# Kernel optimization log

Measured on AMD Instinct MI355X. Metric: run time of the kernel, lower is better.

Reference implementation:

```python
import jax, jax.numpy as jnp
import numpy as np

D_MODEL = 1024
NUM_HEADS = 16
HEAD_DIM = D_MODEL // NUM_HEADS
B, S = 2, 2048
EPS = 1e-8


def setup_inputs() -> dict:
    key = jax.random.key(0)
    ks = jax.random.split(key, 9)
    sc = 1.0 / np.sqrt(D_MODEL)
    return {
        "x": jax.random.normal(ks[0], (B, S, D_MODEL), jnp.float32),
        "wq": jax.random.normal(ks[1], (D_MODEL, D_MODEL), jnp.float32) * sc,
        "bq": jax.random.normal(ks[2], (D_MODEL,), jnp.float32) * 0.01,
        "wk": jax.random.normal(ks[3], (D_MODEL, D_MODEL), jnp.float32) * sc,
        "bk": jax.random.normal(ks[4], (D_MODEL,), jnp.float32) * 0.01,
        "wv": jax.random.normal(ks[5], (D_MODEL, D_MODEL), jnp.float32) * sc,
        "bv": jax.random.normal(ks[6], (D_MODEL,), jnp.float32) * 0.01,
        "wo": jax.random.normal(ks[7], (D_MODEL, D_MODEL), jnp.float32) * sc,
        "bo": jax.random.normal(ks[8], (D_MODEL,), jnp.float32) * 0.01,
    }


def reference(x, wq, bq, wk, bk, wv, bv, wo, bo):
    b, s, d = x.shape
    h, hd = NUM_HEADS, HEAD_DIM
    # projections (torch Linear: y = x W^T + b); reshape to [b, h, s, hd]
    def proj(w, bias):
        return (jnp.einsum('bsd,ed->bse', x, w) + bias).reshape(b, s, h, hd).transpose(0, 2, 1, 3)
    q = proj(wq, bq)
    k = proj(wk, bk)
    v = proj(wv, bv)
    scores = jnp.einsum('bhqd,bhkd->bhqk', q, k) / np.sqrt(hd)
    attn = jax.nn.softmax(scores, axis=-1)
    o = jnp.einsum('bhqk,bhkd->bhqd', attn, v)  # [b, h, s, hd]
    # per-position, per-head Gram-Schmidt exclusion: remove component of o[i]
    # along v[i] (the loop in the original is independent over positions)
    v_norm_sq = jnp.sum(v * v, axis=-1, keepdims=True)          # [b,h,s,1]
    align = jnp.sum(o * v, axis=-1, keepdims=True) / (v_norm_sq + EPS)
    o = o - align * v
    o = o.transpose(0, 2, 1, 3).reshape(b, s, d)
    return jnp.einsum('bsd,ed->bse', o, wo) + bo
```

## Files before the change

kernel.cpp:

```cpp
#include <hip/hip_runtime.h>
#include <stdint.h>

#define SEQ 2048
#define NTOK 4096
#define DM 1024

typedef __bf16 bf16x8 __attribute__((ext_vector_type(8)));
typedef __bf16 bf16x4 __attribute__((ext_vector_type(4)));
typedef float f32x4 __attribute__((ext_vector_type(4)));

__device__ __forceinline__ unsigned short f2bf(float f) {
  union { float f; unsigned u; } v; v.f = f;
  return (unsigned short)((v.u + 0x7fffu + ((v.u >> 16) & 1u)) >> 16);
}
__device__ __forceinline__ float bf2f(unsigned short s) {
  union { unsigned u; float f; } v; v.u = ((unsigned)s) << 16; return v.f;
}
__device__ __forceinline__ unsigned pkbf(float a, float b) {
  union { float f; unsigned u; } x, y; x.f = a; y.f = b;
  return __builtin_amdgcn_perm(y.u + 0x8000u, x.u + 0x8000u, 0x07060302u);
}

__device__ __forceinline__ void async16(const unsigned short* g, unsigned short* l) {
  __builtin_amdgcn_global_load_lds(
      (const __attribute__((address_space(1))) void*)g,
      (__attribute__((address_space(3))) void*)l, 16, 0, 0);
}

__global__ __launch_bounds__(256) void cast_all(
    const float* __restrict__ x, const float* __restrict__ wq,
    const float* __restrict__ wk, const float* __restrict__ wv,
    const float* __restrict__ wo, unsigned short* __restrict__ dst) {
  size_t i = ((size_t)blockIdx.x * 256 + threadIdx.x) * 4;
  const float* src; size_t off;
  if (i < (size_t)NTOK * DM) { src = x; off = i; }
  else {
    size_t j = i - (size_t)NTOK * DM;
    int s = (int)(j >> 20);
    src = (s == 0) ? wq : (s == 1) ? wk : (s == 2) ? wv : wo;
    off = j & 1048575u;
  }
  float4 f = *(const float4*)(src + off);
  ushort4 o;
  o.x = f2bf(f.x); o.y = f2bf(f.y); o.z = f2bf(f.z); o.w = f2bf(f.w);
  *(ushort4*)(dst + i) = o;
}


template<int MI>
__device__ __forceinline__ void stage_half(
    const unsigned short* __restrict__ A, const unsigned short* __restrict__ Bw,
    int m0, int n0, int kt, unsigned short* As, unsigned short* Bs) {
  const int tid = threadIdx.x;
  const int r = tid >> 2, c = tid & 3;
#pragma unroll
  for (int b = 0; b < MI / 2; ++b) {
    const int row = b * 64 + r;
    async16(A + (size_t)(m0 + row) * 1024 + kt + ((c ^ (row & 3)) << 3),
            As + row * 32 + c * 8);
  }
#pragma unroll
  for (int b = 0; b < 2; ++b) {
    const int row = b * 64 + r;
    async16(Bw + (size_t)(n0 + row) * 1024 + kt + ((c ^ (row & 3)) << 3),
            Bs + row * 32 + c * 8);
  }
}

__device__ __forceinline__ void pipe_bar0() {
  asm volatile("s_waitcnt vmcnt(0)\ns_barrier" ::: "memory");
}
template<int MI>
__device__ __forceinline__ void pipe_barN() {
  if constexpr (MI == 4) asm volatile("s_waitcnt vmcnt(4)\ns_barrier" ::: "memory");
  else                   asm volatile("s_waitcnt vmcnt(3)\ns_barrier" ::: "memory");
}

template<int MI>
__device__ __forceinline__ void gemm_pipe(
    const unsigned short* __restrict__ A, const unsigned short* __restrict__ Bw,
    int m0, int n0, f32x4 (&acc)[MI][4],
    unsigned short* AsBase, unsigned short* BsBase) {
  const int tid = threadIdx.x, lane = tid & 63, w = tid >> 6;
  const int wm16 = (w >> 1) * MI * 16, wn = (w & 1) * 64;
  const int quad = lane >> 4, l16 = lane & 15;
  constexpr int ASZ = MI * 32 * 32;
  constexpr int BSZ = 128 * 32;

  stage_half<MI>(A, Bw, m0, n0, 0,  AsBase,       BsBase);
  stage_half<MI>(A, Bw, m0, n0, 32, AsBase + ASZ, BsBase + BSZ);
  pipe_barN<MI>();

  int cur = 0;
  for (int p = 0; p < 32; ++p) {
    const unsigned short* As = AsBase + cur * ASZ;
    const unsigned short* Bs = BsBase + cur * BSZ;

    bf16x8 af[MI], bf[4];
    const int swz = ((quad ^ (l16 & 3)) << 3);
#pragma unroll
    for (int i = 0; i < MI; ++i)
      af[i] = *(const bf16x8*)(As + (wm16 + i * 16 + l16) * 32 + swz);
#pragma unroll
    for (int j = 0; j < 4; ++j)
      bf[j] = *(const bf16x8*)(Bs + (wn + j * 16 + l16) * 32 + swz);

    if (p + 2 < 32) {
      const int slot = (cur == 0) ? 2 : cur - 1;
      stage_half<MI>(A, Bw, m0, n0, (p + 2) * 32,
                     AsBase + slot * ASZ, BsBase + slot * BSZ);
    }

#pragma unroll
    for (int i = 0; i < MI; ++i)
#pragma unroll
      for (int j = 0; j < 4; ++j)
        acc[i][j] = __builtin_amdgcn_mfma_f32_16x16x32_bf16(af[i], bf[j], acc[i][j], 0, 0, 0);

    if (p < 30)       pipe_barN<MI>();
    else if (p == 30) pipe_bar0();
    cur = (cur == 2) ? 0 : cur + 1;
  }
}

__global__ __launch_bounds__(256, 3) void qkv_gemm(
    const unsigned short* __restrict__ xb,
    const unsigned short* __restrict__ wqb, const unsigned short* __restrict__ wkb,
    const unsigned short* __restrict__ wvb,
    const float* __restrict__ bq, const float* __restrict__ bk, const float* __restrict__ bv,
    unsigned short* __restrict__ Q, unsigned short* __restrict__ Kd,
    unsigned short* __restrict__ Vt) {
  __shared__ unsigned short As[3 * 128 * 32], Bs[3 * 128 * 32];
  const int gx = blockIdx.x;
  const int kind = gx >> 8;
  const int rr = gx & 255;
  const int tok = 4 * (rr & 7) + ((rr >> 3) & 3);
  const int oth = rr >> 5;
  const unsigned short* A; const unsigned short* Bw;
  int m0, n0;
  if (kind == 2) { A = wvb; Bw = xb; m0 = oth * 128; n0 = tok * 128; }
  else { A = xb; Bw = kind ? wkb : wqb; m0 = tok * 128; n0 = oth * 128; }

  f32x4 acc[4][4];
#pragma unroll
  for (int i = 0; i < 4; ++i)
#pragma unroll
    for (int j = 0; j < 4; ++j) { f32x4 z = {0.f, 0.f, 0.f, 0.f}; acc[i][j] = z; }
  gemm_pipe<4>(A, Bw, m0, n0, acc, As, Bs);

  const int lane = threadIdx.x & 63, w = threadIdx.x >> 6;
  const int quad = lane >> 4, l16 = lane & 15;
  const int wm = (w >> 1) * 64, wn = (w & 1) * 64;

  if (kind == 2) {
#pragma unroll
    for (int i = 0; i < 4; ++i)
#pragma unroll
      for (int j = 0; j < 4; ++j) {
        const int n = n0 + wn + j * 16 + l16;
        const int tb = n >> 11, s = n & 2047;
#pragma unroll
        for (int r = 0; r < 4; ++r) {
          const int m = m0 + wm + i * 16 + quad * 4 + r;
          const int h = m >> 6, d = m & 63;
          Vt[((size_t)(tb * 16 + h) * 64 + d) * SEQ + s] = f2bf(acc[i][j][r] + bv[m]);
        }
      }
  } else {
    const float* bias = (kind == 0) ? bq : bk;
    const float scale = (kind == 0) ? 0.180336880f : 1.0f;
#pragma unroll
    for (int i = 0; i < 4; ++i)
#pragma unroll
    for (int j = 0; j < 4; ++j) {
        const int col = n0 + wn + j * 16 + l16;
        const float bb = bias[col];
        const int h = col >> 6, d = col & 63;
#pragma unroll
        for (int r = 0; r < 4; ++r) {
          const int m = m0 + wm + i * 16 + quad * 4 + r;
          const int b = m >> 11, s = m & 2047;
          const int bh = b * 16 + h;
          const unsigned short val = f2bf((acc[i][j][r] + bb) * scale);
          if (kind == 0) Q[((size_t)bh * SEQ + s) * 64 + d] = val;
          else           Kd[((size_t)bh * SEQ + s) * 64 + d] = val;
        }
      }
  }
}

__global__ __launch_bounds__(256, 2) void attn_kernel(
    const unsigned short* __restrict__ Q, const unsigned short* __restrict__ Kd,
    const unsigned short* __restrict__ Vt,
    unsigned short* __restrict__ O) {
  __shared__ unsigned short SH[32768];
#define KKB(g, b) (SH + ((g) * 2 + (b)) * 4096)
#define VVB(g, b) (SH + 16384 + ((g) * 2 + (b)) * 4096)
  const int gx = blockIdx.x;
  const int xcd = gx & 7;
  const int idx = gx >> 3;
  const int bh  = xcd * 4 + (idx & 3);
  const int q0  = (idx >> 2) * 128;
  const int tid = threadIdx.x, lane = tid & 63, w = tid >> 6;
  const int kp = w >> 1;
  const int wq = w & 1;
  const int quad = lane >> 4, l16 = lane & 15;
  const unsigned short* Qp = Q + (size_t)bh * SEQ * 64;
  const unsigned short* Kp = Kd + (size_t)bh * SEQ * 64;
  const unsigned short* Vp = Vt + (size_t)bh * 64 * SEQ;
  const int srow = tid >> 3;
  const int sc = ((tid & 7) ^ ((srow & 3) | ((srow & 8) >> 1))) << 3;

#pragma unroll
  for (int c = 0; c < 4; ++c)
    async16(Qp + (size_t)(q0 + c * 32 + srow) * 64 + sc,
            KKB(0, c >> 1) + (c & 1) * 2048 + tid * 8);
  __syncthreads();

  const int gl = (l16 & 3) | ((l16 & 8) >> 1);
  const int sel = l16 & 7;
  const unsigned short* Qsrc = KKB(0, wq);
  bf16x8 bQ[4][2];
#pragma unroll
  for (int qq = 0; qq < 4; ++qq) {
    const int qrow = qq * 16 + l16;
#pragma unroll
    for (int hh = 0; hh < 2; ++hh)
      bQ[qq][hh] = *(const bf16x8*)(Qsrc + qrow * 64 + (((hh * 4 + quad) ^ gl) << 3));
  }
  __syncthreads();

  auto stageKV = [&](int it_, int nb) {
#pragma unroll
    for (int g = 0; g < 2; ++g) {
      const int kt = g * 1024 + it_ * 64;
      async16(Kp + (size_t)(kt + srow) * 64 + sc, KKB(g, nb) + tid * 8);
      async16(Kp + (size_t)(kt + 32 + srow) * 64 + sc, KKB(g, nb) + 2048 + tid * 8);
      async16(Vp + (size_t)srow * SEQ + kt + sc, VVB(g, nb) + tid * 8);
      async16(Vp + (size_t)(32 + srow) * SEQ + kt + sc, VVB(g, nb) + 2048 + tid * 8);
    }
  };
  stageKV(0, 0);

  union { unsigned short u[8]; bf16x8 v; } one8;
#pragma unroll
  for (int t = 0; t < 8; ++t) one8.u[t] = 0x3F80;
  const bf16x8 aOnes = one8.v;

  f32x4 o_acc[4][4];
  f32x4 l_acc[4];
  const f32x4 zinit = {-12.f, -12.f, -12.f, -12.f};
#pragma unroll
  for (int qq = 0; qq < 4; ++qq) {
    f32x4 z = {0.f, 0.f, 0.f, 0.f};
    l_acc[qq] = z;
#pragma unroll
    for (int dt = 0; dt < 4; ++dt) o_acc[qq][dt] = z;
  }

  for (int it = 0; it < 16; ++it) {
    const int cur = it & 1;
    __syncthreads();
    if (it + 1 < 16) stageKV(it + 1, (it + 1) & 1);
    const unsigned short* Ks = KKB(kp, cur);
    const unsigned short* Vs = VVB(kp, cur);

    __builtin_amdgcn_s_setprio(1);

    bf16x8 bP[4][2];
#pragma unroll
    for (int ee = 0; ee < 4; ++ee) {
      const int G = ee >> 1, e = ee & 1;
      const int R = G * 32 + ((l16 >> 2) << 3) + e * 4 + (l16 & 3);
      const unsigned short* arow = Ks + R * 64;
      bf16x8 a0 = *(const bf16x8*)(arow + ((quad ^ sel) << 3));
      bf16x8 a1 = *(const bf16x8*)(arow + (((4 + quad) ^ sel) << 3));
#pragma unroll
      for (int qq = 0; qq < 4; ++qq) {
        f32x4 z = __builtin_amdgcn_mfma_f32_16x16x32_bf16(a0, bQ[qq][0], zinit, 0, 0, 0);
        z = __builtin_amdgcn_mfma_f32_16x16x32_bf16(a1, bQ[qq][1], z, 0, 0, 0);
        const unsigned u0 = (unsigned)(int)__builtin_fmaf(z[0], 8388608.0f, 1065024977.0f);
        const unsigned u1 = (unsigned)(int)__builtin_fmaf(z[1], 8388608.0f, 1065024977.0f);
        const unsigned u2 = (unsigned)(int)__builtin_fmaf(z[2], 8388608.0f, 1065024977.0f);
        const unsigned u3 = (unsigned)(int)__builtin_fmaf(z[3], 8388608.0f, 1065024977.0f);
        union { unsigned d[4]; bf16x8 v; } pk;
        pk.v = bP[qq][G];
        pk.d[e * 2]     = __builtin_amdgcn_perm(u1, u0, 0x07060302u);
        pk.d[e * 2 + 1] = __builtin_amdgcn_perm(u3, u2, 0x07060302u);
        bP[qq][G] = pk.v;
      }
    }

#pragma unroll
    for (int qq = 0; qq < 4; ++qq)
#pragma unroll
      for (int G = 0; G < 2; ++G)
        l_acc[qq] = __builtin_amdgcn_mfma_f32_16x16x32_bf16(aOnes, bP[qq][G], l_acc[qq], 0, 0, 0);

#pragma unroll
    for (int dt = 0; dt < 4; ++dt) {
      const unsigned short* vbase = Vs + (dt * 16 + l16) * 64;
#pragma unroll
      for (int G = 0; G < 2; ++G) {
        bf16x8 aV = *(const bf16x8*)(vbase + (((G * 4 + quad) ^ gl) << 3));
#pragma unroll
        for (int qq = 0; qq < 4; ++qq)
          o_acc[qq][dt] = __builtin_amdgcn_mfma_f32_16x16x32_bf16(aV, bP[qq][G], o_acc[qq][dt], 0, 0, 0);
      }
    }

    __builtin_amdgcn_s_setprio(0);
  }

  __syncthreads();
  float* xf = (float*)SH;
  if (kp == 1) {
    float* dst = xf + (size_t)(wq * 64 + lane) * 68;
#pragma unroll
    for (int qq = 0; qq < 4; ++qq)
#pragma unroll
      for (int dt = 0; dt < 4; ++dt)
        *(f32x4*)(dst + qq * 16 + dt * 4) = o_acc[qq][dt];
    f32x4 lv = {l_acc[0][0], l_acc[1][0], l_acc[2][0], l_acc[3][0]};
    *(f32x4*)(dst + 64) = lv;
  }
  __syncthreads();
  if (kp == 0) {
    const float* src = xf + (size_t)(wq * 64 + lane) * 68;
#pragma unroll
    for (int qq = 0; qq < 4; ++qq)
#pragma unroll
      for (int dt = 0; dt < 4; ++dt)
        o_acc[qq][dt] += *(const f32x4*)(src + qq * 16 + dt * 4);
    const f32x4 lv = *(const f32x4*)(src + 64);

    const int b = bh >> 4, h = bh & 15;
#pragma unroll
    for (int qq = 0; qq < 4; ++qq) {
      const int qg = q0 + wq * 64 + qq * 16 + l16;
      const float inv = 1.0f / (l_acc[qq][0] + lv[qq]);
      const unsigned short* vp = Vp + qg;
      float ov = 0.f, v2 = 0.f;
#pragma unroll
      for (int dt = 0; dt < 4; ++dt)
#pragma unroll
        for (int r = 0; r < 4; ++r) {
          const int d = dt * 16 + quad * 4 + r;
          const float v = bf2f(vp[(size_t)d * SEQ]);
          ov += o_acc[qq][dt][r] * v;
          v2 += v * v;
        }
      ov *= inv;
      ov += __shfl_xor(ov, 16); ov += __shfl_xor(ov, 32);
      v2 += __shfl_xor(v2, 16); v2 += __shfl_xor(v2, 32);
      const float align = ov / (v2 + 1e-8f);
      unsigned short* dst = O + (size_t)(b * SEQ + qg) * DM + h * 64;
#pragma unroll
      for (int dt = 0; dt < 4; ++dt) {
        float a[4];
#pragma unroll
        for (int r = 0; r < 4; ++r) {
          const int d = dt * 16 + quad * 4 + r;
          const float v = bf2f(vp[(size_t)d * SEQ]);
          a[r] = __builtin_fmaf(o_acc[qq][dt][r], inv, -align * v);
        }
        uint2 pk2;
        pk2.x = pkbf(a[0], a[1]);
        pk2.y = pkbf(a[2], a[3]);
        *(uint2*)(dst + dt * 16 + quad * 4) = pk2;
      }
    }
  }
#undef KKB
#undef VVB
}

__global__ __launch_bounds__(256, 3) void out_gemm(
    const unsigned short* __restrict__ Ob, const unsigned short* __restrict__ wob,
    const float* __restrict__ bo, float* __restrict__ out) {
  __shared__ unsigned short As[3 * 128 * 32], Bs[3 * 128 * 32];
  const int m0 = blockIdx.y * 128, n0 = blockIdx.x * 128;
  f32x4 acc[4][4];
#pragma unroll
  for (int i = 0; i < 4; ++i)
#pragma unroll
    for (int j = 0; j < 4; ++j) { f32x4 z = {0.f, 0.f, 0.f, 0.f}; acc[i][j] = z; }

  gemm_pipe<4>(Ob, wob, m0, n0, acc, As, Bs);

  const int lane = threadIdx.x & 63, w = threadIdx.x >> 6;
  const int quad = lane >> 4, l16 = lane & 15;
  const int wm = (w >> 1) * 64, wn = (w & 1) * 64;
#pragma unroll
  for (int i = 0; i < 4; ++i)
#pragma unroll
    for (int j = 0; j < 4; ++j) {
      const int col = n0 + wn + j * 16 + l16;
      const float bb = bo[col];
#pragma unroll
      for (int r = 0; r < 4; ++r) {
        const int m = m0 + wm + i * 16 + quad * 4 + r;
        out[(size_t)m * DM + col] = acc[i][j][r] + bb;
      }
    }
}

extern "C" void kernel_launch(void* const* d_in, const int* in_sizes, int n_in,
                              void* d_out, int out_size, void* d_ws, size_t ws_size,
                              hipStream_t stream) {
  const float* x  = (const float*)d_in[0];
  const float* wq = (const float*)d_in[1];
  const float* bq = (const float*)d_in[2];
  const float* wk = (const float*)d_in[3];
  const float* bk = (const float*)d_in[4];
  const float* wv = (const float*)d_in[5];
  const float* bv = (const float*)d_in[6];
  const float* wo = (const float*)d_in[7];
  const float* bo = (const float*)d_in[8];
  float* out = (float*)d_out;
  (void)in_sizes; (void)n_in; (void)out_size; (void)ws_size;

  unsigned short* ws  = (unsigned short*)d_ws;
  unsigned short* xb  = ws;
  unsigned short* wqb = xb + (size_t)NTOK * DM;
  unsigned short* wkb = wqb + (size_t)DM * DM;
  unsigned short* wvb = wkb + (size_t)DM * DM;
  unsigned short* wob = wvb + (size_t)DM * DM;
  unsigned short* Qb  = wob + (size_t)DM * DM;
  unsigned short* Kb  = Qb + (size_t)NTOK * DM;
  unsigned short* Vtb = Kb + (size_t)NTOK * DM;
  unsigned short* Ob  = Vtb + (size_t)NTOK * DM;

  cast_all<<<8192, 256, 0, stream>>>(x, wq, wk, wv, wo, ws);
  qkv_gemm<<<768, 256, 0, stream>>>(xb, wqb, wkb, wvb, bq, bk, bv, Qb, Kb, Vtb);
  attn_kernel<<<512, 256, 0, stream>>>(Qb, Kb, Vtb, Ob);
  out_gemm<<<dim3(8, 32), 256, 0, stream>>>(Ob, wob, bo, out);
}
```

Baseline: 177.9 us.

## Fuse Q and K projections per block and halve out_gemm M-tile

The Q and K projection blocks now share each staged x tile and compute both outputs with two accumulator sets, so x is loaded once for Q and K. The V blocks run as before, bringing qkv_gemm down to 512 blocks at occupancy 2. out_gemm uses 64-row tiles, doubling its grid to 512 blocks so more CUs are busy. The trade-off is higher register and LDS pressure in the fused QK blocks, and an uneven per-block workload between the QK and V blocks.

```diff
diff --git a/kernel.cpp b/kernel.cpp
--- a/kernel.cpp
+++ b/kernel.cpp
@@ -123,36 +123,132 @@
   }
 }
 
-__global__ __launch_bounds__(256, 3) void qkv_gemm(
+__device__ __forceinline__ void stage_half_qk(
+    const unsigned short* __restrict__ A, const unsigned short* __restrict__ Bq,
+    const unsigned short* __restrict__ Bk,
+    int m0, int n0, int kt, unsigned short* As, unsigned short* Bqs,
+    unsigned short* Bks) {
+  const int tid = threadIdx.x;
+  const int r = tid >> 2, c = tid & 3;
+#pragma unroll
+  for (int b = 0; b < 2; ++b) {
+    const int row = b * 64 + r;
+    const int off = kt + ((c ^ (row & 3)) << 3);
+    async16(A + (size_t)(m0 + row) * 1024 + off, As + row * 32 + c * 8);
+    async16(Bq + (size_t)(n0 + row) * 1024 + off, Bqs + row * 32 + c * 8);
+    async16(Bk + (size_t)(n0 + row) * 1024 + off, Bks + row * 32 + c * 8);
+  }
+}
+__device__ __forceinline__ void pipe_barQK() {
+  asm volatile("s_waitcnt vmcnt(6)\ns_barrier" ::: "memory");
+}
+
+__device__ __forceinline__ void gemm_pipe_qk(
+    const unsigned short* __restrict__ A, const unsigned short* __restrict__ Bq,
+    const unsigned short* __restrict__ Bk,
+    int m0, int n0, f32x4 (&accQ)[4][4], f32x4 (&accK)[4][4],
+    unsigned short* AsBase, unsigned short* BqBase, unsigned short* BkBase) {
+  const int tid = threadIdx.x, lane = tid & 63, w = tid >> 6;
+  const int wm16 = (w >> 1) * 64, wn = (w & 1) * 64;
+  const int quad = lane >> 4, l16 = lane & 15;
+  constexpr int SZ = 128 * 32;
+
+  stage_half_qk(A, Bq, Bk, m0, n0, 0,  AsBase,      BqBase,      BkBase);
+  stage_half_qk(A, Bq, Bk, m0, n0, 32, AsBase + SZ, BqBase + SZ, BkBase + SZ);
+  pipe_barQK();
+
+  int cur = 0;
+  for (int p = 0; p < 32; ++p) {
+    const unsigned short* As = AsBase + cur * SZ;
+    const unsigned short* Bqs = BqBase + cur * SZ;
+    const unsigned short* Bks = BkBase + cur * SZ;
+
+    bf16x8 af[4], bq[4], bk[4];
+    const int swz = ((quad ^ (l16 & 3)) << 3);
+#pragma unroll
+    for (int i = 0; i < 4; ++i)
+      af[i] = *(const bf16x8*)(As + (wm16 + i * 16 + l16) * 32 + swz);
+#pragma unroll
+    for (int j = 0; j < 4; ++j) {
+      bq[j] = *(const bf16x8*)(Bqs + (wn + j * 16 + l16) * 32 + swz);
+      bk[j] = *(const bf16x8*)(Bks + (wn + j * 16 + l16) * 32 + swz);
+    }
+
+    if (p + 2 < 32) {
+      const int slot = (cur == 0) ? 2 : cur - 1;
+      stage_half_qk(A, Bq, Bk, m0, n0, (p + 2) * 32,
+                    AsBase + slot * SZ, BqBase + slot * SZ, BkBase + slot * SZ);
+    }
+
+#pragma unroll
+    for (int i = 0; i < 4; ++i)
+#pragma unroll
+      for (int j = 0; j < 4; ++j) {
+        accQ[i][j] = __builtin_amdgcn_mfma_f32_16x16x32_bf16(af[i], bq[j], accQ[i][j], 0, 0, 0);
+        accK[i][j] = __builtin_amdgcn_mfma_f32_16x16x32_bf16(af[i], bk[j], accK[i][j], 0, 0, 0);
+      }
+
+    if (p < 30)       pipe_barQK();
+    else if (p == 30) pipe_bar0();
+    cur = (cur == 2) ? 0 : cur + 1;
+  }
+}
+
+__global__ __launch_bounds__(256, 2) void qkv_gemm(
     const unsigned short* __restrict__ xb,
     const unsigned short* __restrict__ wqb, const unsigned short* __restrict__ wkb,
     const unsigned short* __restrict__ wvb,
     const float* __restrict__ bq, const float* __restrict__ bk, const float* __restrict__ bv,
     unsigned short* __restrict__ Q, unsigned short* __restrict__ Kd,
     unsigned short* __restrict__ Vt) {
-  __shared__ unsigned short As[3 * 128 * 32], Bs[3 * 128 * 32];
+  __shared__ unsigned short SH[9 * 128 * 32];
   const int gx = blockIdx.x;
-  const int kind = gx >> 8;
   const int rr = gx & 255;
   const int tok = 4 * (rr & 7) + ((rr >> 3) & 3);
   const int oth = rr >> 5;
-  const unsigned short* A; const unsigned short* Bw;
-  int m0, n0;
-  if (kind == 2) { A = wvb; Bw = xb; m0 = oth * 128; n0 = tok * 128; }
-  else { A = xb; Bw = kind ? wkb : wqb; m0 = tok * 128; n0 = oth * 128; }
-
-  f32x4 acc[4][4];
-#pragma unroll
-  for (int i = 0; i < 4; ++i)
-#pragma unroll
-    for (int j = 0; j < 4; ++j) { f32x4 z = {0.f, 0.f, 0.f, 0.f}; acc[i][j] = z; }
-  gemm_pipe<4>(A, Bw, m0, n0, acc, As, Bs);
-
   const int lane = threadIdx.x & 63, w = threadIdx.x >> 6;
   const int quad = lane >> 4, l16 = lane & 15;
   const int wm = (w >> 1) * 64, wn = (w & 1) * 64;
 
-  if (kind == 2) {
+  if (gx < 256) {
+    const int m0 = tok * 128, n0 = oth * 128;
+    f32x4 accQ[4][4], accK[4][4];
+#pragma unroll
+    for (int i = 0; i < 4; ++i)
+#pragma unroll
+      for (int j = 0; j < 4; ++j) {
+        f32x4 z = {0.f, 0.f, 0.f, 0.f};
+        accQ[i][j] = z; accK[i][j] = z;
+      }
+    gemm_pipe_qk(xb, wqb, wkb, m0, n0, accQ, accK,
+                 SH, SH + 3 * 4096, SH + 6 * 4096);
+
+#pragma unroll
+    for (int i = 0; i < 4; ++i)
+#pragma unroll
+      for (int j = 0; j < 4; ++j) {
+        const int col = n0 + wn + j * 16 + l16;
+        const float bbq = bq[col], bbk = bk[col];
+        const int h = col >> 6, d = col & 63;
+#pragma unroll
+        for (int r = 0; r < 4; ++r) {
+          const int m = m0 + wm + i * 16 + quad * 4 + r;
+          const int b = m >> 11, s = m & 2047;
+          const int bh = b * 16 + h;
+          Q[((size_t)bh * SEQ + s) * 64 + d] =
+              f2bf((accQ[i][j][r] + bbq) * 0.180336880f);
+          Kd[((size_t)bh * SEQ + s) * 64 + d] = f2bf(accK[i][j][r] + bbk);
+        }
+      }
+  } else {
+    const int m0 = oth * 128, n0 = tok * 128;
+    f32x4 acc[4][4];
+#pragma unroll
+    for (int i = 0; i < 4; ++i)
+#pragma unroll
+      for (int j = 0; j < 4; ++j) { f32x4 z = {0.f, 0.f, 0.f, 0.f}; acc[i][j] = z; }
+    gemm_pipe<4>(wvb, xb, m0, n0, acc, SH, SH + 3 * 4096);
+
 #pragma unroll
     for (int i = 0; i < 4; ++i)
 #pragma unroll
@@ -164,26 +260,6 @@
           const int m = m0 + wm + i * 16 + quad * 4 + r;
           const int h = m >> 6, d = m & 63;
           Vt[((size_t)(tb * 16 + h) * 64 + d) * SEQ + s] = f2bf(acc[i][j][r] + bv[m]);
-        }
-      }
-  } else {
-    const float* bias = (kind == 0) ? bq : bk;
-    const float scale = (kind == 0) ? 0.180336880f : 1.0f;
-#pragma unroll
-    for (int i = 0; i < 4; ++i)
-#pragma unroll
-    for (int j = 0; j < 4; ++j) {
-        const int col = n0 + wn + j * 16 + l16;
-        const float bb = bias[col];
-        const int h = col >> 6, d = col & 63;
-#pragma unroll
-        for (int r = 0; r < 4; ++r) {
-          const int m = m0 + wm + i * 16 + quad * 4 + r;
-          const int b = m >> 11, s = m & 2047;
-          const int bh = b * 16 + h;
-          const unsigned short val = f2bf((acc[i][j][r] + bb) * scale);
-          if (kind == 0) Q[((size_t)bh * SEQ + s) * 64 + d] = val;
-          else           Kd[((size_t)bh * SEQ + s) * 64 + d] = val;
         }
       }
   }
@@ -375,24 +451,24 @@
 #undef VVB
 }
 
-__global__ __launch_bounds__(256, 3) void out_gemm(
+__global__ __launch_bounds__(256) void out_gemm(
     const unsigned short* __restrict__ Ob, const unsigned short* __restrict__ wob,
     const float* __restrict__ bo, float* __restrict__ out) {
-  __shared__ unsigned short As[3 * 128 * 32], Bs[3 * 128 * 32];
-  const int m0 = blockIdx.y * 128, n0 = blockIdx.x * 128;
-  f32x4 acc[4][4];
-#pragma unroll
-  for (int i = 0; i < 4; ++i)
+  __shared__ unsigned short As[3 * 64 * 32], Bs[3 * 128 * 32];
+  const int m0 = blockIdx.y * 64, n0 = blockIdx.x * 128;
+  f32x4 acc[2][4];
+#pragma unroll
+  for (int i = 0; i < 2; ++i)
 #pragma unroll
     for (int j = 0; j < 4; ++j) { f32x4 z = {0.f, 0.f, 0.f, 0.f}; acc[i][j] = z; }
 
-  gemm_pipe<4>(Ob, wob, m0, n0, acc, As, Bs);
+  gemm_pipe<2>(Ob, wob, m0, n0, acc, As, Bs);
 
   const int lane = threadIdx.x & 63, w = threadIdx.x >> 6;
   const int quad = lane >> 4, l16 = lane & 15;
-  const int wm = (w >> 1) * 64, wn = (w & 1) * 64;
-#pragma unroll
-  for (int i = 0; i < 4; ++i)
+  const int wm = (w >> 1) * 32, wn = (w & 1) * 64;
+#pragma unroll
+  for (int i = 0; i < 2; ++i)
 #pragma unroll
     for (int j = 0; j < 4; ++j) {
       const int col = n0 + wn + j * 16 + l16;
@@ -432,7 +508,7 @@
   unsigned short* Ob  = Vtb + (size_t)NTOK * DM;
 
   cast_all<<<8192, 256, 0, stream>>>(x, wq, wk, wv, wo, ws);
-  qkv_gemm<<<768, 256, 0, stream>>>(xb, wqb, wkb, wvb, bq, bk, bv, Qb, Kb, Vtb);
+  qkv_gemm<<<512, 256, 0, stream>>>(xb, wqb, wkb, wvb, bq, bk, bv, Qb, Kb, Vtb);
   attn_kernel<<<512, 256, 0, stream>>>(Qb, Kb, Vtb, Ob);
-  out_gemm<<<dim3(8, 32), 256, 0, stream>>>(Ob, wob, bo, out);
-}
+  out_gemm<<<dim3(8, 64), 256, 0, stream>>>(Ob, wob, bo, out);
+}
```

New measurement: 177.7 us. Within noise of the previous version (-0.1%).
